# Performance work log

Measured on AMD Instinct MI355X. Metric: run time of the kernel, lower is better.

Reference implementation:

```python
import jax, jax.numpy as jnp
import numpy as np


def _lstm_layer(x_sbi, w_ih, w_hh, b):
    """Custom LSTM layer with elu candidate/cell activations.
    x_sbi: [S, B, I]; w_ih: [4H, I]; w_hh: [4H, H]; b: [4H]. Gate order i,f,g,o.
    Returns outputs [S, B, H].
    """
    H = w_hh.shape[1]
    S, B, _ = x_sbi.shape
    # Precompute the input projection for all timesteps at once.
    xw = jnp.einsum('sbi,gi->sbg', x_sbi, w_ih) + b  # [S, B, 4H]

    def step(carry, xt):
        h, c = carry
        gates = xt + h @ w_hh.T  # [B, 4H]
        i = jax.nn.sigmoid(gates[:, 0 * H:1 * H])
        f = jax.nn.sigmoid(gates[:, 1 * H:2 * H])
        g = jax.nn.elu(gates[:, 2 * H:3 * H])      # custom cell activation
        o = jax.nn.sigmoid(gates[:, 3 * H:4 * H])
        c = f * c + i * g
        h = o * jax.nn.elu(c)                       # custom hidden activation
        return (h, c), h

    h0 = jnp.zeros((B, H), dtype=x_sbi.dtype)
    c0 = jnp.zeros((B, H), dtype=x_sbi.dtype)
    _, out = jax.lax.scan(step, (h0, c0), xw)
    return out  # [S, B, H]


def setup_inputs() -> dict:
    key = jax.random.key(0)
    ks = jax.random.split(key, 12)
    B, S, I, H = 256, 512, 64, 512
    s_in = 1.0 / np.sqrt(H)
    d = {
        'x': jax.random.normal(ks[0], (B, S, I), dtype=jnp.float32),
        'w_ih1': jax.random.normal(ks[1], (4 * H, I), dtype=jnp.float32) * s_in,
        'w_hh1': jax.random.normal(ks[2], (4 * H, H), dtype=jnp.float32) * s_in,
        'b1': jax.random.normal(ks[3], (4 * H,), dtype=jnp.float32) * s_in,
        'w_ih2': jax.random.normal(ks[4], (4 * H, H), dtype=jnp.float32) * s_in,
        'w_hh2': jax.random.normal(ks[5], (4 * H, H), dtype=jnp.float32) * s_in,
        'b2': jax.random.normal(ks[6], (4 * H,), dtype=jnp.float32) * s_in,
        'w_ih3': jax.random.normal(ks[7], (4 * H, H), dtype=jnp.float32) * s_in,
        'w_hh3': jax.random.normal(ks[8], (4 * H, H), dtype=jnp.float32) * s_in,
        'b3': jax.random.normal(ks[9], (4 * H,), dtype=jnp.float32) * s_in,
        'fc_w': jax.random.normal(ks[10], (1, H), dtype=jnp.float32) * s_in,
        'fc_b': jax.random.normal(ks[11], (1,), dtype=jnp.float32) * s_in,
    }
    return d


def reference(x, w_ih1, w_hh1, b1, w_ih2, w_hh2, b2, w_ih3, w_hh3, b3, fc_w, fc_b):
    # x: [B, S, I] -> seq-first [S, B, I] (matches torch permute(1,0,2))
    out = jnp.transpose(x, (1, 0, 2))
    out = _lstm_layer(out, w_ih1, w_hh1, b1)  # dropout = identity (eval)
    out = _lstm_layer(out, w_ih2, w_hh2, b2)
    out = _lstm_layer(out, w_ih3, w_hh3, b3)
    last = out[-1]                             # [B, H]
    return last @ fc_w.T + fc_b                # [B, 1]
```

## Files before the change

kernel.cpp:

```cpp
#include <hip/hip_runtime.h>
#include <stdint.h>
#include <stddef.h>

#define S_LEN 512
#define BATCH 256
#define NIN   64
#define HD    512
#define G4    2048
#define RING_D 32
#define BT    64

typedef _Float16 f16;
typedef _Float16 f16x8 __attribute__((ext_vector_type(8)));
typedef float    f32x4 __attribute__((ext_vector_type(4)));
typedef uint32_t u32x4 __attribute__((ext_vector_type(4)));

__global__ void k_f32_to_f16(const float* __restrict__ src, f16* __restrict__ dst, int n) {
  int i = blockIdx.x * 256 + threadIdx.x;
  if (i < n) dst[i] = (f16)src[i];
}

__global__ void k_x_transpose(const float* __restrict__ x, f16* __restrict__ xin) {
  int idx = blockIdx.x * 256 + threadIdx.x;
  int i  = idx & 63;
  int sb = idx >> 6;
  int b  = sb & 255;
  int s  = sb >> 8;
  xin[idx] = (f16)x[((size_t)b * S_LEN + s) * NIN + i];
}

__global__ void k_zero_i32(uint32_t* p, int n) {
  int i = blockIdx.x * 256 + threadIdx.x;
  if (i < n) p[i] = 0u;
}

__global__ __launch_bounds__(512, 2) void k_fused(
    const f16* __restrict__ whh,
    const f16* __restrict__ wih,
    const float* __restrict__ b0,
    const float* __restrict__ b1,
    const float* __restrict__ b2,
    const f16* __restrict__ xin,
    f16* __restrict__ ring,
    int* __restrict__ flags,
    f16* __restrict__ hlast) {
  const int tid  = threadIdx.x;
  const int lane = tid & 63;
  const int wave = tid >> 6;
  const int bidx = blockIdx.x;
  const int l    = bidx >> 6;
  const int bi   = (bidx >> 4) & 3;
  const int gi   = bidx & 15;
  const int ln   = lane & 15;
  const int quad = lane >> 4;

  __shared__ __align__(16) char smem[131072];
  char* lh_b  = smem;
  char* lhp_b = smem + 65536;
  float* lgate = (float*)smem;

  auto swz = [](int row, int boff) { return row * 1024 + (boff ^ ((row & 7) << 4)); };

  const f16* whh_l = whh + (size_t)l * G4 * HD;
  const f16* wih_l = wih + (size_t)l * G4 * HD;
  const float* bias_l = (l == 0) ? b0 : (l == 1 ? b1 : b2);

  const int grow = (wave >> 1) * HD + gi * 32 + (wave & 1) * 16 + ln;
  f16x8 wfh[16];
#pragma unroll
  for (int ks = 0; ks < 16; ks++) {
    u32x4 t = *(const u32x4*)(whh_l + (size_t)grow * HD + ks * 32 + quad * 8);
    asm volatile("" : "+v"(t));
    wfh[ks] = __builtin_bit_cast(f16x8, t);
  }
  f16x8 wfi[16];
  if (l == 0) {
#pragma unroll
    for (int ks = 0; ks < 2; ks++) {
      u32x4 t = *(const u32x4*)(wih_l + (size_t)grow * NIN + ks * 32 + quad * 8);
      asm volatile("" : "+v"(t));
      wfi[ks] = __builtin_bit_cast(f16x8, t);
    }
  } else {
#pragma unroll
    for (int ks = 0; ks < 16; ks++) {
      u32x4 t = *(const u32x4*)(wih_l + (size_t)grow * HD + ks * 32 + quad * 8);
      asm volatile("" : "+v"(t));
      wfi[ks] = __builtin_bit_cast(f16x8, t);
    }
  }

  const int brow = tid >> 5;
  const int hl_  = tid & 31;
  float cv[4] = {0.f, 0.f, 0.f, 0.f};
  const float bv0 = bias_l[0 * HD + gi * 32 + hl_];
  const float bv1 = bias_l[1 * HD + gi * 32 + hl_];
  const float bv2 = bias_l[2 * HD + gi * 32 + hl_];
  const float bv3 = bias_l[3 * HD + gi * 32 + hl_];

  int* fown = flags + l * 64 + bi * 16;
  int* myflag = fown + gi;
  const int* fprev = (l > 0) ? (flags + (l - 1) * 64 + bi * 16) : fown;
  const int* fnext = (l < 2) ? (flags + (l + 1) * 64 + bi * 16) : fown;

  for (int t = 0; t < S_LEN; t++) {
    u32x4 xv = {};
    if (l == 0) {
      const int xr = tid >> 3, xc = tid & 7;
      xv = *(const u32x4*)(xin + ((size_t)(t * 256 + bi * BT + xr)) * NIN + xc * 8);
    }

    if (wave == 0) {
      const int* fp = fown;
      int need = t;
      if (quad == 1 && l > 0)      { fp = fprev; need = t + 1; }
      else if (quad == 2 && l < 2) { fp = fnext; need = t + 2 - RING_D; }
      int v = __hip_atomic_load(fp + ln, __ATOMIC_RELAXED, __HIP_MEMORY_SCOPE_AGENT);
      while (!__all(v >= need)) {
        __builtin_amdgcn_s_sleep(1);
        v = __hip_atomic_load(fp + ln, __ATOMIC_RELAXED, __HIP_MEMORY_SCOPE_AGENT);
      }
    }
    __syncthreads();

    const uint64_t* hown = (const uint64_t*)(ring
        + ((size_t)l * RING_D + (t & (RING_D - 1))) * (BATCH * HD)
        + (size_t)(bi * BT) * HD);
    uint64_t dA[16];
#pragma unroll
    for (int j = 0; j < 16; j++)
      dA[j] = __hip_atomic_load(hown + j * 512 + tid, __ATOMIC_RELAXED, __HIP_MEMORY_SCOPE_AGENT);

    if (l > 0) {
      const uint64_t* hprev = (const uint64_t*)(ring
          + ((size_t)(l - 1) * RING_D + ((t + 1) & (RING_D - 1))) * (BATCH * HD)
          + (size_t)(bi * BT) * HD);
      uint64_t dB[16];
#pragma unroll
      for (int j = 0; j < 16; j++)
        dB[j] = __hip_atomic_load(hprev + j * 512 + tid, __ATOMIC_RELAXED, __HIP_MEMORY_SCOPE_AGENT);
#pragma unroll
      for (int j = 0; j < 16; j++) {
        const int e = j * 512 + tid, row = e >> 7, c8 = e & 127;
        *(uint64_t*)(lhp_b + swz(row, c8 * 8)) = dB[j];
      }
    } else {
      const int xr = tid >> 3, xc = tid & 7;
      *(u32x4*)(lhp_b + swz(xr, xc * 16)) = xv;
    }
#pragma unroll
    for (int j = 0; j < 16; j++) {
      const int e = j * 512 + tid, row = e >> 7, c8 = e & 127;
      *(uint64_t*)(lh_b + swz(row, c8 * 8)) = dA[j];
    }
    __syncthreads();

    f32x4 acc[4] = {};
#pragma unroll
    for (int ks = 0; ks < 16; ks++) {
#pragma unroll
      for (int mi = 0; mi < 4; mi++) {
        const f16x8 af = *(const f16x8*)(lh_b + swz(mi * 16 + ln, ks * 64 + quad * 16));
        acc[mi] = __builtin_amdgcn_mfma_f32_16x16x32_f16(af, wfh[ks], acc[mi], 0, 0, 0);
      }
    }
    if (l == 0) {
#pragma unroll
      for (int ks = 0; ks < 2; ks++) {
#pragma unroll
        for (int mi = 0; mi < 4; mi++) {
          const f16x8 ap = *(const f16x8*)(lhp_b + swz(mi * 16 + ln, ks * 64 + quad * 16));
          acc[mi] = __builtin_amdgcn_mfma_f32_16x16x32_f16(ap, wfi[ks], acc[mi], 0, 0, 0);
        }
      }
    } else {
#pragma unroll
      for (int ks = 0; ks < 16; ks++) {
#pragma unroll
        for (int mi = 0; mi < 4; mi++) {
          const f16x8 ap = *(const f16x8*)(lhp_b + swz(mi * 16 + ln, ks * 64 + quad * 16));
          acc[mi] = __builtin_amdgcn_mfma_f32_16x16x32_f16(ap, wfi[ks], acc[mi], 0, 0, 0);
        }
      }
    }
    __syncthreads();

    const int gcol = (wave >> 1) * 32 + (wave & 1) * 16 + ln;
#pragma unroll
    for (int mi = 0; mi < 4; mi++)
#pragma unroll
      for (int rr = 0; rr < 4; rr++)
        lgate[(mi * 16 + quad * 4 + rr) * 128 + gcol] = acc[mi][rr];
    __syncthreads();

    f16* hout = ring + ((size_t)l * RING_D + ((t + 1) & (RING_D - 1))) * (BATCH * HD);
#pragma unroll
    for (int s = 0; s < 4; s++) {
      const int row = brow + s * 16;
      float g0 = lgate[row * 128 + 0  + hl_] + bv0;
      float g1 = lgate[row * 128 + 32 + hl_] + bv1;
      float g2 = lgate[row * 128 + 64 + hl_] + bv2;
      float g3 = lgate[row * 128 + 96 + hl_] + bv3;
      const float igt = 1.f / (1.f + expf(-g0));
      const float fgt = 1.f / (1.f + expf(-g1));
      const float ggt = g2 > 0.f ? g2 : expm1f(g2);
      const float ogt = 1.f / (1.f + expf(-g3));
      cv[s] = fgt * cv[s] + igt * ggt;
      const float hv = ogt * (cv[s] > 0.f ? cv[s] : expm1f(cv[s]));
      f16 hv16 = (f16)hv;
      unsigned short us;
      __builtin_memcpy(&us, &hv16, 2);
      const size_t col = (size_t)(bi * BT + row) * HD + gi * 32 + hl_;
      __hip_atomic_store((unsigned short*)(hout + col), us,
                         __ATOMIC_RELAXED, __HIP_MEMORY_SCOPE_AGENT);
      if (l == 2 && t == S_LEN - 1) hlast[col] = hv16;
    }
    __syncthreads();
    if (tid == 0)
      __hip_atomic_store(myflag, t + 1, __ATOMIC_RELAXED, __HIP_MEMORY_SCOPE_AGENT);
  }
}

__global__ __launch_bounds__(64) void k_fc(const f16* __restrict__ hlast,
                                           const float* __restrict__ fcw,
                                           const float* __restrict__ fcb,
                                           float* __restrict__ out) {
  const int b = blockIdx.x, lane = threadIdx.x;
  const f16* hp = hlast + (size_t)b * HD + lane * 8;
  float s = 0.f;
#pragma unroll
  for (int j = 0; j < 8; j++) s += (float)hp[j] * fcw[lane * 8 + j];
  for (int off = 32; off; off >>= 1) s += __shfl_down(s, off);
  if (lane == 0) out[b] = s + fcb[0];
}

extern "C" void kernel_launch(void* const* d_in, const int* in_sizes, int n_in,
                              void* d_out, int out_size, void* d_ws, size_t ws_size,
                              hipStream_t stream) {
  (void)in_sizes; (void)n_in; (void)out_size; (void)ws_size;
  const float* x      = (const float*)d_in[0];
  const float* wih[3] = {(const float*)d_in[1], (const float*)d_in[4], (const float*)d_in[7]};
  const float* whh[3] = {(const float*)d_in[2], (const float*)d_in[5], (const float*)d_in[8]};
  const float* bia[3] = {(const float*)d_in[3], (const float*)d_in[6], (const float*)d_in[9]};
  const float* fcw = (const float*)d_in[10];
  const float* fcb = (const float*)d_in[11];
  float* out = (float*)d_out;

  char* ws = (char*)d_ws;
  size_t off = 0;
  auto alloc = [&](size_t bytes) -> char* {
    off = (off + 255) & ~(size_t)255;
    char* p = ws + off;
    off += bytes;
    return p;
  };

  f16* xin   = (f16*)alloc((size_t)S_LEN * BATCH * NIN * 2);
  f16* wih16 = (f16*)alloc((size_t)3 * G4 * HD * 2);
  f16* whh16 = (f16*)alloc((size_t)3 * G4 * HD * 2);
  f16* ring  = (f16*)alloc((size_t)3 * RING_D * BATCH * HD * 2);
  int* flags = (int*)alloc(256 * 4);
  f16* hlast = (f16*)alloc((size_t)BATCH * HD * 2);

  {
    int n = S_LEN * BATCH * NIN;
    k_x_transpose<<<dim3(n / 256), dim3(256), 0, stream>>>(x, xin);
  }
  k_f32_to_f16<<<dim3((G4 * NIN + 255) / 256), dim3(256), 0, stream>>>(wih[0], wih16, G4 * NIN);
  k_f32_to_f16<<<dim3((G4 * HD + 255) / 256), dim3(256), 0, stream>>>(wih[1], wih16 + (size_t)G4 * HD, G4 * HD);
  k_f32_to_f16<<<dim3((G4 * HD + 255) / 256), dim3(256), 0, stream>>>(wih[2], wih16 + (size_t)2 * G4 * HD, G4 * HD);
  for (int l = 0; l < 3; l++)
    k_f32_to_f16<<<dim3((G4 * HD + 255) / 256), dim3(256), 0, stream>>>(whh[l], whh16 + (size_t)l * G4 * HD, G4 * HD);
  for (int l = 0; l < 3; l++)
    k_zero_i32<<<dim3(BATCH * HD / 2 / 256), dim3(256), 0, stream>>>(
        (uint32_t*)(ring + (size_t)l * RING_D * BATCH * HD), BATCH * HD / 2);
  k_zero_i32<<<dim3(1), dim3(256), 0, stream>>>((uint32_t*)flags, 192);

  k_fused<<<dim3(192), dim3(512), 0, stream>>>(whh16, wih16, bia[0], bia[1], bia[2],
                                               xin, ring, flags, hlast);

  k_fc<<<dim3(BATCH), dim3(64), 0, stream>>>(hlast, fcw, fcb, out);
}
```

Baseline: 5.836 ms.

## Split K across waves by weight matrix, drop flag-wait barrier, swizzle gate LDS

Each wave now covers 32 gate columns and uses only one weight matrix: even waves handle the recurrent W_hh and odd waves the input W_ih. Each A fragment read from LDS is reused across two MFMAs, and the two partial sums are added during the gate epilogue. All waves now poll the flags themselves instead of wave 0 followed by a barrier. Global-to-LDS copies use 128-bit stores, the gate scratch is XOR-swizzled to avoid bank conflicts, and sigmoid uses fast __expf. On layer 0 the odd waves have only 2 k-steps while even waves have 16, so the work is imbalanced there, and the extra polling adds memory traffic.

```diff
diff --git a/kernel.cpp b/kernel.cpp
--- a/kernel.cpp
+++ b/kernel.cpp
@@ -14,6 +14,7 @@
 typedef _Float16 f16x8 __attribute__((ext_vector_type(8)));
 typedef float    f32x4 __attribute__((ext_vector_type(4)));
 typedef uint32_t u32x4 __attribute__((ext_vector_type(4)));
+typedef uint64_t u64x2 __attribute__((ext_vector_type(2)));
 
 __global__ void k_f32_to_f16(const float* __restrict__ src, f16* __restrict__ dst, int n) {
   int i = blockIdx.x * 256 + threadIdx.x;
@@ -47,17 +48,19 @@
   const int tid  = threadIdx.x;
   const int lane = tid & 63;
   const int wave = tid >> 6;
-  const int bidx = blockIdx.x;
-  const int l    = bidx >> 6;
-  const int bi   = (bidx >> 4) & 3;
-  const int gi   = bidx & 15;
+  const int l    = blockIdx.x >> 6;
+  const int bi   = (blockIdx.x >> 4) & 3;
+  const int gi   = blockIdx.x & 15;
   const int ln   = lane & 15;
   const int quad = lane >> 4;
+  const int g    = wave >> 1;
+  const int kh   = wave & 1;
 
   __shared__ __align__(16) char smem[131072];
-  char* lh_b  = smem;
-  char* lhp_b = smem + 65536;
-  float* lgate = (float*)smem;
+  char*  lh_b  = smem;
+  char*  lhp_b = smem + 65536;
+  float* lg0   = (float*)smem;
+  float* lg1   = (float*)(smem + 32768);
 
   auto swz = [](int row, int boff) { return row * 1024 + (boff ^ ((row & 7) << 4)); };
 
@@ -65,28 +68,29 @@
   const f16* wih_l = wih + (size_t)l * G4 * HD;
   const float* bias_l = (l == 0) ? b0 : (l == 1 ? b1 : b2);
 
-  const int grow = (wave >> 1) * HD + gi * 32 + (wave & 1) * 16 + ln;
-  f16x8 wfh[16];
-#pragma unroll
-  for (int ks = 0; ks < 16; ks++) {
-    u32x4 t = *(const u32x4*)(whh_l + (size_t)grow * HD + ks * 32 + quad * 8);
-    asm volatile("" : "+v"(t));
-    wfh[ks] = __builtin_bit_cast(f16x8, t);
-  }
-  f16x8 wfi[16];
-  if (l == 0) {
-#pragma unroll
-    for (int ks = 0; ks < 2; ks++) {
-      u32x4 t = *(const u32x4*)(wih_l + (size_t)grow * NIN + ks * 32 + quad * 8);
-      asm volatile("" : "+v"(t));
-      wfi[ks] = __builtin_bit_cast(f16x8, t);
+  f16x8 wf[16][2];
+  if (kh == 0 || l > 0) {
+    const f16* W = kh ? wih_l : whh_l;
+#pragma unroll
+    for (int nb = 0; nb < 2; nb++) {
+      const int r = g * 512 + gi * 32 + nb * 16 + ln;
+#pragma unroll
+      for (int ks = 0; ks < 16; ks++) {
+        u32x4 tmp = *(const u32x4*)(W + (size_t)r * HD + ks * 32 + quad * 8);
+        asm volatile("" : "+v"(tmp));
+        wf[ks][nb] = __builtin_bit_cast(f16x8, tmp);
+      }
     }
   } else {
 #pragma unroll
-    for (int ks = 0; ks < 16; ks++) {
-      u32x4 t = *(const u32x4*)(wih_l + (size_t)grow * HD + ks * 32 + quad * 8);
-      asm volatile("" : "+v"(t));
-      wfi[ks] = __builtin_bit_cast(f16x8, t);
+    for (int nb = 0; nb < 2; nb++) {
+      const int r = g * 512 + gi * 32 + nb * 16 + ln;
+#pragma unroll
+      for (int ks = 0; ks < 2; ks++) {
+        u32x4 tmp = *(const u32x4*)(wih_l + (size_t)r * NIN + ks * 32 + quad * 8);
+        asm volatile("" : "+v"(tmp));
+        wf[ks][nb] = __builtin_bit_cast(f16x8, tmp);
+      }
     }
   }
 
@@ -104,13 +108,7 @@
   const int* fnext = (l < 2) ? (flags + (l + 1) * 64 + bi * 16) : fown;
 
   for (int t = 0; t < S_LEN; t++) {
-    u32x4 xv = {};
-    if (l == 0) {
-      const int xr = tid >> 3, xc = tid & 7;
-      xv = *(const u32x4*)(xin + ((size_t)(t * 256 + bi * BT + xr)) * NIN + xc * 8);
-    }
-
-    if (wave == 0) {
+    {
       const int* fp = fown;
       int need = t;
       if (quad == 1 && l > 0)      { fp = fprev; need = t + 1; }
@@ -121,90 +119,106 @@
         v = __hip_atomic_load(fp + ln, __ATOMIC_RELAXED, __HIP_MEMORY_SCOPE_AGENT);
       }
     }
-    __syncthreads();
+    asm volatile("" ::: "memory");
 
     const uint64_t* hown = (const uint64_t*)(ring
         + ((size_t)l * RING_D + (t & (RING_D - 1))) * (BATCH * HD)
         + (size_t)(bi * BT) * HD);
-    uint64_t dA[16];
-#pragma unroll
-    for (int j = 0; j < 16; j++)
-      dA[j] = __hip_atomic_load(hown + j * 512 + tid, __ATOMIC_RELAXED, __HIP_MEMORY_SCOPE_AGENT);
-
+    uint64_t a0[8], a1[8];
+#pragma unroll
+    for (int j = 0; j < 8; j++) {
+      a0[j] = __hip_atomic_load(hown + j * 1024 + tid * 2,     __ATOMIC_RELAXED, __HIP_MEMORY_SCOPE_AGENT);
+      a1[j] = __hip_atomic_load(hown + j * 1024 + tid * 2 + 1, __ATOMIC_RELAXED, __HIP_MEMORY_SCOPE_AGENT);
+    }
     if (l > 0) {
       const uint64_t* hprev = (const uint64_t*)(ring
           + ((size_t)(l - 1) * RING_D + ((t + 1) & (RING_D - 1))) * (BATCH * HD)
           + (size_t)(bi * BT) * HD);
-      uint64_t dB[16];
-#pragma unroll
-      for (int j = 0; j < 16; j++)
-        dB[j] = __hip_atomic_load(hprev + j * 512 + tid, __ATOMIC_RELAXED, __HIP_MEMORY_SCOPE_AGENT);
-#pragma unroll
-      for (int j = 0; j < 16; j++) {
-        const int e = j * 512 + tid, row = e >> 7, c8 = e & 127;
-        *(uint64_t*)(lhp_b + swz(row, c8 * 8)) = dB[j];
+      uint64_t p0[8], p1[8];
+#pragma unroll
+      for (int j = 0; j < 8; j++) {
+        p0[j] = __hip_atomic_load(hprev + j * 1024 + tid * 2,     __ATOMIC_RELAXED, __HIP_MEMORY_SCOPE_AGENT);
+        p1[j] = __hip_atomic_load(hprev + j * 1024 + tid * 2 + 1, __ATOMIC_RELAXED, __HIP_MEMORY_SCOPE_AGENT);
+      }
+#pragma unroll
+      for (int j = 0; j < 8; j++) {
+        const int e = j * 1024 + tid * 2, row = e >> 7, c8 = e & 127;
+        u64x2 p; p[0] = p0[j]; p[1] = p1[j];
+        *(u64x2*)(lhp_b + swz(row, c8 * 8)) = p;
       }
     } else {
       const int xr = tid >> 3, xc = tid & 7;
+      u32x4 xv = *(const u32x4*)(xin + ((size_t)(t * 256 + bi * BT + xr)) * NIN + xc * 8);
       *(u32x4*)(lhp_b + swz(xr, xc * 16)) = xv;
     }
 #pragma unroll
-    for (int j = 0; j < 16; j++) {
-      const int e = j * 512 + tid, row = e >> 7, c8 = e & 127;
-      *(uint64_t*)(lh_b + swz(row, c8 * 8)) = dA[j];
-    }
-    __syncthreads();
-
-    f32x4 acc[4] = {};
-#pragma unroll
-    for (int ks = 0; ks < 16; ks++) {
-#pragma unroll
-      for (int mi = 0; mi < 4; mi++) {
-        const f16x8 af = *(const f16x8*)(lh_b + swz(mi * 16 + ln, ks * 64 + quad * 16));
-        acc[mi] = __builtin_amdgcn_mfma_f32_16x16x32_f16(af, wfh[ks], acc[mi], 0, 0, 0);
-      }
-    }
-    if (l == 0) {
+    for (int j = 0; j < 8; j++) {
+      const int e = j * 1024 + tid * 2, row = e >> 7, c8 = e & 127;
+      u64x2 p; p[0] = a0[j]; p[1] = a1[j];
+      *(u64x2*)(lh_b + swz(row, c8 * 8)) = p;
+    }
+    __syncthreads();
+
+    f32x4 acc[4][2] = {};
+    const char* tb = kh ? lhp_b : lh_b;
+    if (kh == 0 || l > 0) {
+#pragma unroll
+      for (int ks = 0; ks < 16; ks++) {
+        f16x8 af[4];
+#pragma unroll
+        for (int mi = 0; mi < 4; mi++)
+          af[mi] = *(const f16x8*)(tb + swz(mi * 16 + ln, ks * 64 + quad * 16));
+#pragma unroll
+        for (int mi = 0; mi < 4; mi++)
+#pragma unroll
+          for (int nb = 0; nb < 2; nb++)
+            acc[mi][nb] = __builtin_amdgcn_mfma_f32_16x16x32_f16(af[mi], wf[ks][nb], acc[mi][nb], 0, 0, 0);
+      }
+    } else {
 #pragma unroll
       for (int ks = 0; ks < 2; ks++) {
-#pragma unroll
-        for (int mi = 0; mi < 4; mi++) {
-          const f16x8 ap = *(const f16x8*)(lhp_b + swz(mi * 16 + ln, ks * 64 + quad * 16));
-          acc[mi] = __builtin_amdgcn_mfma_f32_16x16x32_f16(ap, wfi[ks], acc[mi], 0, 0, 0);
-        }
-      }
-    } else {
-#pragma unroll
-      for (int ks = 0; ks < 16; ks++) {
-#pragma unroll
-        for (int mi = 0; mi < 4; mi++) {
-          const f16x8 ap = *(const f16x8*)(lhp_b + swz(mi * 16 + ln, ks * 64 + quad * 16));
-          acc[mi] = __builtin_amdgcn_mfma_f32_16x16x32_f16(ap, wfi[ks], acc[mi], 0, 0, 0);
-        }
-      }
-    }
-    __syncthreads();
-
-    const int gcol = (wave >> 1) * 32 + (wave & 1) * 16 + ln;
-#pragma unroll
-    for (int mi = 0; mi < 4; mi++)
-#pragma unroll
-      for (int rr = 0; rr < 4; rr++)
-        lgate[(mi * 16 + quad * 4 + rr) * 128 + gcol] = acc[mi][rr];
+        f16x8 af[4];
+#pragma unroll
+        for (int mi = 0; mi < 4; mi++)
+          af[mi] = *(const f16x8*)(tb + swz(mi * 16 + ln, ks * 64 + quad * 16));
+#pragma unroll
+        for (int mi = 0; mi < 4; mi++)
+#pragma unroll
+          for (int nb = 0; nb < 2; nb++)
+            acc[mi][nb] = __builtin_amdgcn_mfma_f32_16x16x32_f16(af[mi], wf[ks][nb], acc[mi][nb], 0, 0, 0);
+      }
+    }
+    __syncthreads();
+
+    {
+      float* lg = kh ? lg1 : lg0;
+#pragma unroll
+      for (int mi = 0; mi < 4; mi++)
+#pragma unroll
+        for (int nb = 0; nb < 2; nb++)
+#pragma unroll
+          for (int rr = 0; rr < 4; rr++) {
+            const int row = mi * 16 + quad * 4 + rr;
+            const int col = g * 32 + nb * 16 + ln;
+            lg[row * 128 + (col ^ (((row >> 2) & 7) << 2))] = acc[mi][nb][rr];
+          }
+    }
     __syncthreads();
 
     f16* hout = ring + ((size_t)l * RING_D + ((t + 1) & (RING_D - 1))) * (BATCH * HD);
 #pragma unroll
     for (int s = 0; s < 4; s++) {
       const int row = brow + s * 16;
-      float g0 = lgate[row * 128 + 0  + hl_] + bv0;
-      float g1 = lgate[row * 128 + 32 + hl_] + bv1;
-      float g2 = lgate[row * 128 + 64 + hl_] + bv2;
-      float g3 = lgate[row * 128 + 96 + hl_] + bv3;
-      const float igt = 1.f / (1.f + expf(-g0));
-      const float fgt = 1.f / (1.f + expf(-g1));
+      const int xm = ((row >> 2) & 7) << 2;
+      const int rb = row * 128;
+      float g0 = lg0[rb + ((0  + hl_) ^ xm)] + lg1[rb + ((0  + hl_) ^ xm)] + bv0;
+      float g1 = lg0[rb + ((32 + hl_) ^ xm)] + lg1[rb + ((32 + hl_) ^ xm)] + bv1;
+      float g2 = lg0[rb + ((64 + hl_) ^ xm)] + lg1[rb + ((64 + hl_) ^ xm)] + bv2;
+      float g3 = lg0[rb + ((96 + hl_) ^ xm)] + lg1[rb + ((96 + hl_) ^ xm)] + bv3;
+      const float igt = 1.f / (1.f + __expf(-g0));
+      const float fgt = 1.f / (1.f + __expf(-g1));
       const float ggt = g2 > 0.f ? g2 : expm1f(g2);
-      const float ogt = 1.f / (1.f + expf(-g3));
+      const float ogt = 1.f / (1.f + __expf(-g3));
       cv[s] = fgt * cv[s] + igt * ggt;
       const float hv = ogt * (cv[s] > 0.f ? cv[s] : expm1f(cv[s]));
       f16 hv16 = (f16)hv;
```

After: 5.788 ms. Within noise of the previous version (-0.8%).
